# Performance work log

Measured on AMD Instinct MI355X. Metric: run time of the kernel, lower is better.

The kernel has to match this reference:

```python
import jax, jax.numpy as jnp
import numpy as np

FP8_MAX = 448.0  # float8_e4m3fn max
EPS = 1e-6
H = 4096
T = 16384


def _rmsnorm(x, w, eps=EPS):
    # vLLM RMSNorm: x * rsqrt(mean(x^2) + eps) * weight, computed in fp32
    ms = jnp.mean(x * x, axis=-1, keepdims=True)
    return x * jax.lax.rsqrt(ms + eps) * w


def _fp8_linear_dyn(y, w_t, wscale):
    # per-token dynamic fp8 quant: scale = max|y| / 448, quantize, fp8 GEMM, dequant
    s = jnp.max(jnp.abs(y), axis=-1, keepdims=True) / FP8_MAX  # [T,1]
    s = jnp.maximum(s, 1e-10)
    q = jnp.clip(y / s, -FP8_MAX, FP8_MAX)
    q = q.astype(jnp.float8_e4m3fn).astype(jnp.float32)  # snap to fp8 grid
    out = q @ w_t                                         # [T,H]
    return out * s * wscale[:, 0]                          # per-token * per-out-channel


def setup_inputs() -> dict:
    key = jax.random.key(0)
    ks = jax.random.split(key, 9)
    x = jax.random.uniform(ks[0], (T, H), dtype=jnp.float32)
    # RMSNorm weights (init ones in vLLM; perturb for a nontrivial baseline)
    nw0 = 1.0 + 0.1 * jax.random.normal(ks[1], (H,), dtype=jnp.float32)
    nw1 = 1.0 + 0.1 * jax.random.normal(ks[2], (H,), dtype=jnp.float32)
    nw2 = 1.0 + 0.1 * jax.random.normal(ks[3], (H,), dtype=jnp.float32)
    # fp8 weights: rand(H,H) snapped to e4m3 grid, transposed (y @ W.T)
    def fp8_w(k):
        w = jax.random.uniform(k, (H, H), dtype=jnp.float32)
        return w.astype(jnp.float8_e4m3fn).astype(jnp.float32).T
    w0 = fp8_w(ks[4])
    w1 = fp8_w(ks[5])
    ws0 = jax.random.uniform(ks[6], (H, 1), dtype=jnp.float32)
    ws1 = jax.random.uniform(ks[7], (H, 1), dtype=jnp.float32)
    return {"x": x, "nw0": nw0, "nw1": nw1, "nw2": nw2,
            "w0": w0, "w1": w1, "ws0": ws0, "ws1": ws1}


def reference(x, nw0, nw1, nw2, w0, w1, ws0, ws1):
    resid = jnp.sqrt(x)
    y = _rmsnorm(x, nw0)
    x2 = _fp8_linear_dyn(y, w0, ws0)
    # fused add + rmsnorm: residual updated in place semantics
    resid = x2 + resid
    y2 = _rmsnorm(resid, nw1)
    x3 = _fp8_linear_dyn(y2, w1, ws1)
    resid = x3 + resid
    y3 = _rmsnorm(resid, nw2)
    return y3
```

## Files before the change

### kernel.cpp

```cpp
#include <hip/hip_runtime.h>
#include <stdint.h>

#define TT 16384
#define HH 4096

typedef uint8_t u8;
typedef uint32_t u32;
typedef __attribute__((ext_vector_type(16))) float f32x16;
typedef __attribute__((ext_vector_type(8))) int i32x8;

__device__ __forceinline__ u32 cvt4_fp8(float a, float b, float c, float d) {
  u32 v = 0;
  v = __builtin_amdgcn_cvt_pk_fp8_f32(a, b, v, false);
  v = __builtin_amdgcn_cvt_pk_fp8_f32(c, d, v, true);
  return v;
}

__device__ __forceinline__ void gl_lds16(const void* g, void* l) {
  __builtin_amdgcn_global_load_lds(
      (const __attribute__((address_space(1))) void*)g,
      (__attribute__((address_space(3))) void*)l, 16, 0, 0);
}

__device__ __forceinline__ i32x8 ld32B(const u8* p0, const u8* p1) {
  const uint4 a = *(const uint4*)p0;
  const uint4 b = *(const uint4*)p1;
  i32x8 r;
  r[0] = (int)a.x; r[1] = (int)a.y; r[2] = (int)a.z; r[3] = (int)a.w;
  r[4] = (int)b.x; r[5] = (int)b.y; r[6] = (int)b.z; r[7] = (int)b.w;
  return r;
}

__global__ __launch_bounds__(256) void kwquant(const float* __restrict__ w,
                                               u8* __restrict__ wq) {
  __shared__ __align__(16) u8 tile[64][68];
  const int n0 = blockIdx.x * 64;
  const int k0 = blockIdx.y * 64;
  const int t = threadIdx.x;
  const int tr = t >> 4, tc = t & 15;
#pragma unroll
  for (int p = 0; p < 4; ++p) {
    const int kl = p * 16 + tr;
    const float4 v = *(const float4*)(w + (size_t)(k0 + kl) * HH + n0 + tc * 4);
    const u32 pk = cvt4_fp8(v.x, v.y, v.z, v.w);
    tile[tc * 4 + 0][kl] = (u8)(pk);
    tile[tc * 4 + 1][kl] = (u8)(pk >> 8);
    tile[tc * 4 + 2][kl] = (u8)(pk >> 16);
    tile[tc * 4 + 3][kl] = (u8)(pk >> 24);
  }
  __syncthreads();
  const int jr = t >> 2;
  const int kc = (t & 3) * 16;
  uint4 ov;
  ov.x = *(const u32*)&tile[jr][kc + 0];
  ov.y = *(const u32*)&tile[jr][kc + 4];
  ov.z = *(const u32*)&tile[jr][kc + 8];
  ov.w = *(const u32*)&tile[jr][kc + 12];
  *(uint4*)(wq + (size_t)(n0 + jr) * HH + k0 + kc) = ov;
}

__device__ __forceinline__ float wred_sum(float v) {
#pragma unroll
  for (int o = 32; o; o >>= 1) v += __shfl_down(v, o, 64);
  return v;
}
__device__ __forceinline__ float wred_max(float v) {
#pragma unroll
  for (int o = 32; o; o >>= 1) v = fmaxf(v, __shfl_down(v, o, 64));
  return v;
}

template <int MODE>
__global__ __launch_bounds__(256) void knorm(const float* __restrict__ src,
                                             const float* __restrict__ nw,
                                             float* __restrict__ resid_out,
                                             u8* __restrict__ qout,
                                             float* __restrict__ sout,
                                             float* __restrict__ yout) {
  __shared__ float red[4];
  __shared__ float redm[4];
  const int row = blockIdx.x;
  const int t = threadIdx.x;
  const int lane = t & 63, wid = t >> 6;
  const float* rp = src + (size_t)row * HH;

  float4 xv[4];
  float ssq = 0.f;
#pragma unroll
  for (int p = 0; p < 4; ++p) {
    xv[p] = *((const float4*)rp + p * 256 + t);
    ssq += xv[p].x * xv[p].x;
    ssq += xv[p].y * xv[p].y;
    ssq += xv[p].z * xv[p].z;
    ssq += xv[p].w * xv[p].w;
  }
  if (MODE == 0) {
    float* rr = resid_out + (size_t)row * HH;
#pragma unroll
    for (int p = 0; p < 4; ++p) {
      float4 r4;
      r4.x = sqrtf(xv[p].x); r4.y = sqrtf(xv[p].y);
      r4.z = sqrtf(xv[p].z); r4.w = sqrtf(xv[p].w);
      *((float4*)rr + p * 256 + t) = r4;
    }
  }
  ssq = wred_sum(ssq);
  if (lane == 0) red[wid] = ssq;
  __syncthreads();
  const float ms = (((red[0] + red[1]) + red[2]) + red[3]) * (1.0f / HH);
  const float inv = 1.0f / sqrtf(ms + 1e-6f);

  float y[16];
  float amax = 0.f;
#pragma unroll
  for (int p = 0; p < 4; ++p) {
    const float4 wv = *((const float4*)nw + p * 256 + t);
    y[p * 4 + 0] = (xv[p].x * inv) * wv.x;
    y[p * 4 + 1] = (xv[p].y * inv) * wv.y;
    y[p * 4 + 2] = (xv[p].z * inv) * wv.z;
    y[p * 4 + 3] = (xv[p].w * inv) * wv.w;
    amax = fmaxf(amax, fabsf(y[p * 4 + 0]));
    amax = fmaxf(amax, fabsf(y[p * 4 + 1]));
    amax = fmaxf(amax, fabsf(y[p * 4 + 2]));
    amax = fmaxf(amax, fabsf(y[p * 4 + 3]));
  }

  if (MODE == 2) {
    float* yp = yout + (size_t)row * HH;
#pragma unroll
    for (int p = 0; p < 4; ++p) {
      float4 o;
      o.x = y[p * 4 + 0]; o.y = y[p * 4 + 1];
      o.z = y[p * 4 + 2]; o.w = y[p * 4 + 3];
      *((float4*)yp + p * 256 + t) = o;
    }
    return;
  }

  amax = wred_max(amax);
  if (lane == 0) redm[wid] = amax;
  __syncthreads();
  const float bmax = fmaxf(fmaxf(redm[0], redm[1]), fmaxf(redm[2], redm[3]));
  const float sval = fmaxf(bmax / 448.0f, 1e-10f);

  u32* qp = (u32*)(qout + (size_t)row * HH);
#pragma unroll
  for (int p = 0; p < 4; ++p) {
    float q0 = fminf(fmaxf(y[p * 4 + 0] / sval, -448.f), 448.f);
    float q1 = fminf(fmaxf(y[p * 4 + 1] / sval, -448.f), 448.f);
    float q2 = fminf(fmaxf(y[p * 4 + 2] / sval, -448.f), 448.f);
    float q3 = fminf(fmaxf(y[p * 4 + 3] / sval, -448.f), 448.f);
    qp[p * 256 + t] = cvt4_fp8(q0, q1, q2, q3);
  }
  if (t == 0) sout[row] = sval;
}

__global__ __launch_bounds__(256) void kgemm(const u8* __restrict__ Aq,
                                             const u8* __restrict__ Bq,
                                             const float* __restrict__ srow,
                                             const float* __restrict__ wsc,
                                             float* __restrict__ resid) {
  constexpr int K = HH, N = HH;
  constexpr int NT = K / 64;
  __shared__ __align__(16) u8 smAf[3 * 128 * 64];
  __shared__ __align__(16) u8 smBf[3 * 128 * 64];

  const int bidraw = blockIdx.x;
  const int xcd = bidraw & 7;
  const int c = bidraw >> 3;
  const int g = c >> 4;
  const int gr = g >> 3, gc = g & 7;
  const int gm = (c >> 2) & 3, gn = c & 3;
  const int tm = xcd * 16 + gr * 4 + gm;
  const int tn = gc * 4 + gn;
  const int row0 = tm * 128, col0 = tn * 128;

  const int t = threadIdx.x;
  const int lane = t & 63, wid = t >> 6;
  const int wr = wid >> 1, wc = wid & 1;
  const int rl32 = lane & 31, hi = lane >> 5;

  f32x16 acc[2][2];
#pragma unroll
  for (int m = 0; m < 2; ++m)
#pragma unroll
    for (int n = 0; n < 2; ++n) acc[m][n] = (f32x16)0.f;

  int aoffg[2], boffg[2], ldso[2];
#pragma unroll
  for (int p = 0; p < 2; ++p) {
    const int off = (wid * 2 + p) * 1024 + lane * 16;
    const int r = off >> 6;
    const int cb = ((off >> 4) & 3) ^ ((r >> 1) & 3);
    aoffg[p] = (row0 + r) * K + cb * 16;
    boffg[p] = (col0 + r) * K + cb * 16;
    ldso[p] = off;
  }

  int aro[2][2], bro[2][2];
#pragma unroll
  for (int m = 0; m < 2; ++m) {
    const int r = wr * 64 + m * 32 + rl32;
    const int swz = (r >> 1) & 3;
    aro[m][0] = r * 64 + ((hi * 2) ^ swz) * 16;
    aro[m][1] = r * 64 + ((hi * 2 + 1) ^ swz) * 16;
  }
#pragma unroll
  for (int n = 0; n < 2; ++n) {
    const int r = wc * 64 + n * 32 + rl32;
    const int swz = (r >> 1) & 3;
    bro[n][0] = r * 64 + ((hi * 2) ^ swz) * 16;
    bro[n][1] = r * 64 + ((hi * 2 + 1) ^ swz) * 16;
  }

#pragma unroll
  for (int p = 0; p < 2; ++p) {
    gl_lds16(Aq + aoffg[p], smAf + ldso[p]);
    gl_lds16(Bq + boffg[p], smBf + ldso[p]);
  }
#pragma unroll
  for (int p = 0; p < 2; ++p) {
    gl_lds16(Aq + aoffg[p] + 64, smAf + 8192 + ldso[p]);
    gl_lds16(Bq + boffg[p] + 64, smBf + 8192 + ldso[p]);
  }

  int bc = 0;
  int bs = 2;
  for (int it = 0; it < NT; ++it) {
    if (it + 2 < NT) {
      const size_t ko = (size_t)(it + 2) * 64;
      u8* dA = smAf + bs * 8192;
      u8* dB = smBf + bs * 8192;
#pragma unroll
      for (int p = 0; p < 2; ++p) {
        gl_lds16(Aq + aoffg[p] + ko, dA + ldso[p]);
        gl_lds16(Bq + boffg[p] + ko, dB + ldso[p]);
      }
      asm volatile("s_waitcnt vmcnt(8)" ::: "memory");
    } else if (it + 1 < NT) {
      asm volatile("s_waitcnt vmcnt(4)" ::: "memory");
    } else {
      asm volatile("s_waitcnt vmcnt(0)" ::: "memory");
    }
    __builtin_amdgcn_s_barrier();
    __builtin_amdgcn_sched_barrier(0);

    const u8* sA = smAf + bc * 8192;
    const u8* sB = smBf + bc * 8192;
    i32x8 av[2], bv[2];
#pragma unroll
    for (int m = 0; m < 2; ++m) av[m] = ld32B(sA + aro[m][0], sA + aro[m][1]);
#pragma unroll
    for (int n = 0; n < 2; ++n) bv[n] = ld32B(sB + bro[n][0], sB + bro[n][1]);
    __builtin_amdgcn_s_setprio(1);
#pragma unroll
    for (int m = 0; m < 2; ++m)
#pragma unroll
      for (int n = 0; n < 2; ++n)
        acc[m][n] = __builtin_amdgcn_mfma_scale_f32_32x32x64_f8f6f4(
            av[m], bv[n], acc[m][n], 0 , 0 ,
            0, 0x7f7f7f7f, 0, 0x7f7f7f7f);
    __builtin_amdgcn_s_setprio(0);
    __builtin_amdgcn_sched_barrier(0);
    __builtin_amdgcn_s_barrier();
    bc = (bc == 2) ? 0 : bc + 1;
    bs = (bs == 2) ? 0 : bs + 1;
  }

  const int cc = rl32;
  const int rb = hi * 4;
  float wvv[2];
#pragma unroll
  for (int n = 0; n < 2; ++n) wvv[n] = wsc[col0 + wc * 64 + n * 32 + cc];
#pragma unroll
  for (int m = 0; m < 2; ++m) {
#pragma unroll
    for (int g2 = 0; g2 < 4; ++g2) {
#pragma unroll
      for (int j = 0; j < 4; ++j) {
        const int row = row0 + wr * 64 + m * 32 + g2 * 8 + rb + j;
        const float sv = srow[row];
#pragma unroll
        for (int n = 0; n < 2; ++n) {
          const int col = col0 + wc * 64 + n * 32 + cc;
          const size_t idx = (size_t)row * N + col;
          resid[idx] = resid[idx] + (acc[m][n][g2 * 4 + j] * sv) * wvv[n];
        }
      }
    }
  }
}

extern "C" void kernel_launch(void* const* d_in, const int* in_sizes, int n_in,
                              void* d_out, int out_size, void* d_ws, size_t ws_size,
                              hipStream_t stream) {
  const float* x   = (const float*)d_in[0];
  const float* nw0 = (const float*)d_in[1];
  const float* nw1 = (const float*)d_in[2];
  const float* nw2 = (const float*)d_in[3];
  const float* w0  = (const float*)d_in[4];
  const float* w1  = (const float*)d_in[5];
  const float* ws0 = (const float*)d_in[6];
  const float* ws1 = (const float*)d_in[7];
  float* out = (float*)d_out;

  u8* q = (u8*)d_ws;
  u8* w0q = q + (size_t)TT * HH;
  u8* w1q = w0q + (size_t)HH * HH;
  float* sbuf = (float*)(w1q + (size_t)HH * HH);

  dim3 wg(HH / 64, HH / 64);
  kwquant<<<wg, 256, 0, stream>>>(w0, w0q);
  kwquant<<<wg, 256, 0, stream>>>(w1, w1q);

  knorm<0><<<TT, 256, 0, stream>>>(x, nw0, out, q, sbuf, nullptr);
  kgemm<<<(TT / 128) * (HH / 128), 256, 0, stream>>>(q, w0q, sbuf, ws0, out);
  knorm<1><<<TT, 256, 0, stream>>>(out, nw1, nullptr, q, sbuf, nullptr);
  kgemm<<<(TT / 128) * (HH / 128), 256, 0, stream>>>(q, w1q, sbuf, ws1, out);
  knorm<2><<<TT, 256, 0, stream>>>(out, nw2, nullptr, nullptr, nullptr, out);
}
```

Before: 1.045 ms.

## Load GEMM A operand directly from global into registers, bypassing LDS

The fp8 GEMM stops staging the A tile in shared memory. Each lane now loads its 32-byte A fragment straight from global memory into registers, double-buffered across two k-steps, while B keeps the three-stage LDS ring. The loop is unrolled by two with reworked vmcnt waits. This halves LDS traffic and shared memory use but adds uncoalesced per-lane global loads of A, plus more complex wait counting that must stay correct.

```diff
diff --git a/kernel.cpp b/kernel.cpp
--- a/kernel.cpp
+++ b/kernel.cpp
@@ -22,6 +22,19 @@
       (__attribute__((address_space(3))) void*)l, 16, 0, 0);
 }
 
+struct A2 { uint4 lo, hi; };
+__device__ __forceinline__ A2 ldA32(const u8* p) {
+  A2 r;
+  r.lo = ((const uint4*)p)[0];
+  r.hi = ((const uint4*)p)[1];
+  return r;
+}
+__device__ __forceinline__ i32x8 packA(const A2& a) {
+  i32x8 r;
+  r[0] = (int)a.lo.x; r[1] = (int)a.lo.y; r[2] = (int)a.lo.z; r[3] = (int)a.lo.w;
+  r[4] = (int)a.hi.x; r[5] = (int)a.hi.y; r[6] = (int)a.hi.z; r[7] = (int)a.hi.w;
+  return r;
+}
 __device__ __forceinline__ i32x8 ld32B(const u8* p0, const u8* p1) {
   const uint4 a = *(const uint4*)p0;
   const uint4 b = *(const uint4*)p1;
@@ -162,8 +175,7 @@
                                              float* __restrict__ resid) {
   constexpr int K = HH, N = HH;
   constexpr int NT = K / 64;
-  __shared__ __align__(16) u8 smAf[3 * 128 * 64];
-  __shared__ __align__(16) u8 smBf[3 * 128 * 64];
+  __shared__ __align__(16) u8 smB[3 * 128 * 64];
 
   const int bidraw = blockIdx.x;
   const int xcd = bidraw & 7;
@@ -186,25 +198,22 @@
 #pragma unroll
     for (int n = 0; n < 2; ++n) acc[m][n] = (f32x16)0.f;
 
-  int aoffg[2], boffg[2], ldso[2];
+  const u8* apA[2];
+#pragma unroll
+  for (int m = 0; m < 2; ++m)
+    apA[m] = Aq + (size_t)(row0 + wr * 64 + m * 32 + rl32) * K + hi * 32;
+
+  int boffg[2], ldso[2];
 #pragma unroll
   for (int p = 0; p < 2; ++p) {
     const int off = (wid * 2 + p) * 1024 + lane * 16;
     const int r = off >> 6;
     const int cb = ((off >> 4) & 3) ^ ((r >> 1) & 3);
-    aoffg[p] = (row0 + r) * K + cb * 16;
     boffg[p] = (col0 + r) * K + cb * 16;
     ldso[p] = off;
   }
 
-  int aro[2][2], bro[2][2];
-#pragma unroll
-  for (int m = 0; m < 2; ++m) {
-    const int r = wr * 64 + m * 32 + rl32;
-    const int swz = (r >> 1) & 3;
-    aro[m][0] = r * 64 + ((hi * 2) ^ swz) * 16;
-    aro[m][1] = r * 64 + ((hi * 2 + 1) ^ swz) * 16;
-  }
+  int bro[2][2];
 #pragma unroll
   for (int n = 0; n < 2; ++n) {
     const int r = wc * 64 + n * 32 + rl32;
@@ -214,57 +223,87 @@
   }
 
 #pragma unroll
-  for (int p = 0; p < 2; ++p) {
-    gl_lds16(Aq + aoffg[p], smAf + ldso[p]);
-    gl_lds16(Bq + boffg[p], smBf + ldso[p]);
-  }
-#pragma unroll
-  for (int p = 0; p < 2; ++p) {
-    gl_lds16(Aq + aoffg[p] + 64, smAf + 8192 + ldso[p]);
-    gl_lds16(Bq + boffg[p] + 64, smBf + 8192 + ldso[p]);
-  }
+  for (int p = 0; p < 2; ++p) gl_lds16(Bq + boffg[p], smB + ldso[p]);
+#pragma unroll
+  for (int p = 0; p < 2; ++p) gl_lds16(Bq + boffg[p] + 64, smB + 8192 + ldso[p]);
+  A2 a0[2], a1[2];
+#pragma unroll
+  for (int m = 0; m < 2; ++m) a0[m] = ldA32(apA[m]);
 
   int bc = 0;
-  int bs = 2;
-  for (int it = 0; it < NT; ++it) {
+  for (int it = 0; it < NT; it += 2) {
+    const int b_even = bc;
+    const int b_odd = (bc == 2) ? 0 : bc + 1;
+    const int b_st0 = (b_odd == 2) ? 0 : b_odd + 1;
+    const int b_st1 = b_even;
+
+    if (it + 1 < NT) {
+#pragma unroll
+      for (int m = 0; m < 2; ++m) a1[m] = ldA32(apA[m] + (it + 1) * 64);
+    }
     if (it + 2 < NT) {
       const size_t ko = (size_t)(it + 2) * 64;
-      u8* dA = smAf + bs * 8192;
-      u8* dB = smBf + bs * 8192;
-#pragma unroll
-      for (int p = 0; p < 2; ++p) {
-        gl_lds16(Aq + aoffg[p] + ko, dA + ldso[p]);
-        gl_lds16(Bq + boffg[p] + ko, dB + ldso[p]);
-      }
-      asm volatile("s_waitcnt vmcnt(8)" ::: "memory");
-    } else if (it + 1 < NT) {
-      asm volatile("s_waitcnt vmcnt(4)" ::: "memory");
+#pragma unroll
+      for (int p = 0; p < 2; ++p)
+        gl_lds16(Bq + boffg[p] + ko, smB + b_st0 * 8192 + ldso[p]);
+      asm volatile("s_waitcnt vmcnt(12)" ::: "memory");
     } else {
-      asm volatile("s_waitcnt vmcnt(0)" ::: "memory");
+      asm volatile("s_waitcnt vmcnt(10)" ::: "memory");
     }
     __builtin_amdgcn_s_barrier();
     __builtin_amdgcn_sched_barrier(0);
-
-    const u8* sA = smAf + bc * 8192;
-    const u8* sB = smBf + bc * 8192;
-    i32x8 av[2], bv[2];
-#pragma unroll
-    for (int m = 0; m < 2; ++m) av[m] = ld32B(sA + aro[m][0], sA + aro[m][1]);
-#pragma unroll
-    for (int n = 0; n < 2; ++n) bv[n] = ld32B(sB + bro[n][0], sB + bro[n][1]);
-    __builtin_amdgcn_s_setprio(1);
-#pragma unroll
-    for (int m = 0; m < 2; ++m)
-#pragma unroll
-      for (int n = 0; n < 2; ++n)
-        acc[m][n] = __builtin_amdgcn_mfma_scale_f32_32x32x64_f8f6f4(
-            av[m], bv[n], acc[m][n], 0 , 0 ,
-            0, 0x7f7f7f7f, 0, 0x7f7f7f7f);
-    __builtin_amdgcn_s_setprio(0);
+    {
+      const u8* sB = smB + b_even * 8192;
+      const i32x8 bv0 = ld32B(sB + bro[0][0], sB + bro[0][1]);
+      const i32x8 bv1 = ld32B(sB + bro[1][0], sB + bro[1][1]);
+      __builtin_amdgcn_s_setprio(1);
+#pragma unroll
+      for (int m = 0; m < 2; ++m) {
+        const i32x8 av = packA(a0[m]);
+        acc[m][0] = __builtin_amdgcn_mfma_scale_f32_32x32x64_f8f6f4(
+            av, bv0, acc[m][0], 0, 0, 0, 0x7f7f7f7f, 0, 0x7f7f7f7f);
+        acc[m][1] = __builtin_amdgcn_mfma_scale_f32_32x32x64_f8f6f4(
+            av, bv1, acc[m][1], 0, 0, 0, 0x7f7f7f7f, 0, 0x7f7f7f7f);
+      }
+      __builtin_amdgcn_s_setprio(0);
+    }
     __builtin_amdgcn_sched_barrier(0);
     __builtin_amdgcn_s_barrier();
-    bc = (bc == 2) ? 0 : bc + 1;
-    bs = (bs == 2) ? 0 : bs + 1;
+
+    if (it + 2 < NT) {
+#pragma unroll
+      for (int m = 0; m < 2; ++m) a0[m] = ldA32(apA[m] + (it + 2) * 64);
+    }
+    if (it + 3 < NT) {
+      const size_t ko = (size_t)(it + 3) * 64;
+#pragma unroll
+      for (int p = 0; p < 2; ++p)
+        gl_lds16(Bq + boffg[p] + ko, smB + b_st1 * 8192 + ldso[p]);
+      asm volatile("s_waitcnt vmcnt(12)" ::: "memory");
+    } else {
+      asm volatile("s_waitcnt vmcnt(4)" ::: "memory");
+    }
+    __builtin_amdgcn_s_barrier();
+    __builtin_amdgcn_sched_barrier(0);
+    {
+      const u8* sB = smB + b_odd * 8192;
+      const i32x8 bv0 = ld32B(sB + bro[0][0], sB + bro[0][1]);
+      const i32x8 bv1 = ld32B(sB + bro[1][0], sB + bro[1][1]);
+      __builtin_amdgcn_s_setprio(1);
+#pragma unroll
+      for (int m = 0; m < 2; ++m) {
+        const i32x8 av = packA(a1[m]);
+        acc[m][0] = __builtin_amdgcn_mfma_scale_f32_32x32x64_f8f6f4(
+            av, bv0, acc[m][0], 0, 0, 0, 0x7f7f7f7f, 0, 0x7f7f7f7f);
+        acc[m][1] = __builtin_amdgcn_mfma_scale_f32_32x32x64_f8f6f4(
+            av, bv1, acc[m][1], 0, 0, 0, 0x7f7f7f7f, 0, 0x7f7f7f7f);
+      }
+      __builtin_amdgcn_s_setprio(0);
+    }
+    __builtin_amdgcn_sched_barrier(0);
+    __builtin_amdgcn_s_barrier();
+
+    bc = (bc + 2 > 2) ? bc - 1 : bc + 2;
   }
 
   const int cc = rl32;
```

Measured after the change: 1.507 ms. 1.44x slower.
